# Optimization experiments

Hardware: AMD Instinct MI355X
Metric: run time of the kernel (lower is better)

## Reference

```python
import jax, jax.numpy as jnp
import numpy as np

N_NODES = 49
FEAT_DIM = 1280            # efficientnet_v2_s feature dim
NODE_DIM = FEAT_DIM // N_NODES  # 26
GAT_HID = 256
HEADS = 4
NUM_CLASSES = 5
BATCH = 8192


def _grid_edges():
    # 7x7 grid, 8-neighborhood, as in _create_grid_edges, plus PyG default self loops
    edges = []
    for i in range(7):
        for j in range(7):
            node = i * 7 + j
            for di in (-1, 0, 1):
                for dj in (-1, 0, 1):
                    if di == 0 and dj == 0:
                        continue
                    ni, nj = i + di, j + dj
                    if 0 <= ni < 7 and 0 <= nj < 7:
                        edges.append((node, ni * 7 + nj))
    edges += [(n, n) for n in range(N_NODES)]  # add_self_loops=True (PyG default)
    return np.asarray(edges, dtype=np.int64).T  # [2, 361]


def setup_inputs() -> dict:
    key = jax.random.key(0)
    ks = jax.random.split(key, 16)
    s = 0.05
    inp = {
        "x": jax.random.normal(ks[0], (BATCH, FEAT_DIM), jnp.float32),
        "transform_w": jax.random.normal(ks[1], (FEAT_DIM, N_NODES * NODE_DIM), jnp.float32) * s,
        "transform_b": jnp.zeros((N_NODES * NODE_DIM,), jnp.float32),
        # GATv2 layer 1: 26 -> 64 per head, 4 heads, concat -> 256
        "g1_wl": jax.random.normal(ks[2], (NODE_DIM, GAT_HID), jnp.float32) * s,
        "g1_wr": jax.random.normal(ks[3], (NODE_DIM, GAT_HID), jnp.float32) * s,
        "g1_att": jax.random.normal(ks[4], (HEADS, GAT_HID // HEADS), jnp.float32) * s,
        "g1_b": jnp.zeros((GAT_HID,), jnp.float32),
        # GATv2 layer 2: 256 -> 256, 1 head, mean
        "g2_wl": jax.random.normal(ks[5], (GAT_HID, GAT_HID), jnp.float32) * s,
        "g2_wr": jax.random.normal(ks[6], (GAT_HID, GAT_HID), jnp.float32) * s,
        "g2_att": jax.random.normal(ks[7], (1, GAT_HID), jnp.float32) * s,
        "g2_b": jnp.zeros((GAT_HID,), jnp.float32),
        "fc_w": jax.random.normal(ks[8], (NODE_DIM + GAT_HID, NUM_CLASSES), jnp.float32) * s,
        "fc_b": jnp.zeros((NUM_CLASSES,), jnp.float32),
        "edge_index": jnp.asarray(_grid_edges()),
    }
    return inp


def _gatv2(x, src, dst, wl, wr, att, b, heads, out_ch, concat):
    # PyG GATv2Conv (share_weights=False, negative_slope=0.2, eval mode)
    n = x.shape[0]
    xl = (x @ wl).reshape(n, heads, out_ch)  # source messages
    xr = (x @ wr).reshape(n, heads, out_ch)  # target side of attention
    e = jax.nn.leaky_relu(xl[src] + xr[dst], 0.2)        # [E, H, C]
    score = jnp.einsum('ehc,hc->eh', e, att)             # [E, H]
    smax = jax.ops.segment_max(score, dst, num_segments=n)
    ex = jnp.exp(score - smax[dst])
    den = jax.ops.segment_sum(ex, dst, num_segments=n)
    alpha = ex / den[dst]                                # softmax over in-edges per node
    out = jax.ops.segment_sum(xl[src] * alpha[..., None], dst, num_segments=n)  # [N,H,C]
    out = out.reshape(n, heads * out_ch) if concat else out.mean(axis=1)
    return out + b


def reference(x, transform_w, transform_b, g1_wl, g1_wr, g1_att, g1_b,
              g2_wl, g2_wr, g2_att, g2_b, fc_w, fc_b, edge_index):
    src, dst = edge_index[0], edge_index[1]
    node = (x @ transform_w + transform_b).reshape(-1, N_NODES, NODE_DIM)  # [B,49,26]

    def graph(nf):
        h = _gatv2(nf, src, dst, g1_wl, g1_wr, g1_att, g1_b, HEADS, GAT_HID // HEADS, True)
        h = jax.nn.elu(h)  # dropout inactive in eval
        h = _gatv2(h, src, dst, g2_wl, g2_wr, g2_att, g2_b, 1, GAT_HID, False)
        return h  # [49, 256]

    g = jax.vmap(graph)(node)                              # [B,49,256]
    pooled = jnp.concatenate([node, g], axis=-1).mean(axis=1)  # [B, 282]
    return pooled @ fc_w + fc_b
```

## Files before the change

### kernel.cpp

```cpp
#include <hip/hip_runtime.h>
#include <hip/hip_bf16.h>

typedef __bf16 bf16;
typedef __attribute__((ext_vector_type(8))) __bf16 bf16x8;
typedef __attribute__((ext_vector_type(4))) float f32x4;

constexpr int BATCH = 8192, NN = 49, ND = 26, NOUT = 1274, FD = 1280;
constexpr int HID = 256, NE = 361, HEADS = 4;
constexpr int KT_X = 40;
constexpr int MT_X = 512;
constexpr int NB_W = 10;
constexpr int NTB  = 9;

constexpr size_t OFF_XPACK = 0;
constexpr size_t SZ_XPACK  = (size_t)MT_X * KT_X * 512 * 2;
constexpr size_t OFF_WPACK = OFF_XPACK + SZ_XPACK;
constexpr size_t SZ_WPACK  = (size_t)NB_W * NTB * KT_X * 512 * 2;
constexpr size_t OFF_B1    = OFF_WPACK + SZ_WPACK;
constexpr size_t SZ_B1     = (size_t)32 * 512 * 2;
constexpr size_t OFF_B2    = OFF_B1 + SZ_B1;
constexpr size_t SZ_B2     = (size_t)32 * 8 * 512 * 2;
constexpr size_t OFF_N32   = OFF_B2 + SZ_B2;
constexpr size_t SZ_N32    = (size_t)BATCH * NN * 32 * 2;
constexpr size_t OFF_PN    = OFF_N32 + SZ_N32;
constexpr size_t SZ_PN     = (size_t)BATCH * ND * 4;
constexpr size_t OFF_CSR   = OFF_PN + SZ_PN;
constexpr size_t SZ_CSR    = 8192;
constexpr size_t OFF_CHUNK = OFF_CSR + SZ_CSR;


__global__ __launch_bounds__(256) void k_pack_x(const float* __restrict__ x,
                                                bf16* __restrict__ xp) {
    int g = blockIdx.x * 256 + threadIdx.x;
    int lane = g & 63, frag = g >> 6;
    int mt = frag / KT_X, kt = frag - mt * KT_X;
    int row = mt * 16 + (lane & 15);
    int k0  = kt * 32 + (lane >> 4) * 8;
    const float* src = x + (size_t)row * FD + k0;
    bf16x8 v;
#pragma unroll
    for (int j = 0; j < 8; ++j) v[j] = (bf16)src[j];
    *(bf16x8*)(xp + ((size_t)frag * 64 + lane) * 8) = v;
}

__global__ __launch_bounds__(256) void k_pack_w(const float* __restrict__ w,
                                                bf16* __restrict__ wp) {
    int g = blockIdx.x * 256 + threadIdx.x;
    int lane = g & 63, frag = g >> 6;
    int kt = frag % KT_X, t2 = frag / KT_X;
    int nt = t2 % NTB, nb = t2 / NTB;
    int col = nb * 130 + nt * 16 + (lane & 15);
    int k0  = kt * 32 + (lane >> 4) * 8;
    bool ok = (col < NOUT) && (col < nb * 130 + 130);
    bf16x8 v;
#pragma unroll
    for (int j = 0; j < 8; ++j)
        v[j] = ok ? (bf16)w[(size_t)(k0 + j) * NOUT + col] : (bf16)0.f;
    *(bf16x8*)(wp + ((size_t)frag * 64 + lane) * 8) = v;
}

__global__ __launch_bounds__(256) void k_pack_g1(const float* __restrict__ wl,
                                                 const float* __restrict__ wr,
                                                 bf16* __restrict__ bp) {
    int g = blockIdx.x * 256 + threadIdx.x;
    int lane = g & 63, nt = g >> 6;
    int n  = nt * 16 + (lane & 15);
    int k0 = (lane >> 4) * 8;
    bf16x8 v;
#pragma unroll
    for (int j = 0; j < 8; ++j) {
        int k = k0 + j;
        float f = 0.f;
        if (k < ND) f = (n < HID) ? wl[k * HID + n] : wr[k * HID + (n - HID)];
        v[j] = (bf16)f;
    }
    *(bf16x8*)(bp + ((size_t)nt * 64 + lane) * 8) = v;
}

__global__ __launch_bounds__(256) void k_pack_g2(const float* __restrict__ wl,
                                                 const float* __restrict__ wr,
                                                 bf16* __restrict__ bp) {
    int g = blockIdx.x * 256 + threadIdx.x;
    int lane = g & 63, frag = g >> 6;
    int nt = frag >> 3, kt = frag & 7;
    int n  = nt * 16 + (lane & 15);
    int k0 = kt * 32 + (lane >> 4) * 8;
    bf16x8 v;
#pragma unroll
    for (int j = 0; j < 8; ++j) {
        int k = k0 + j;
        float f = (n < HID) ? wl[k * HID + n] : wr[k * HID + (n - HID)];
        v[j] = (bf16)f;
    }
    *(bf16x8*)(bp + ((size_t)frag * 64 + lane) * 8) = v;
}

__global__ __launch_bounds__(128) void k_csr_par(const int* __restrict__ ei,
                                                 int* __restrict__ csr) {
    __shared__ int es[NE], ed[NE], cnt[NN], ocnt[NN], off[NN + 1], ooff[NN + 1];
    int tid = threadIdx.x;
    if (tid < NN) { cnt[tid] = 0; ocnt[tid] = 0; }
    for (int e = tid; e < NE; e += 128) { es[e] = ei[e]; ed[e] = ei[NE + e]; }
    __syncthreads();
    for (int e = tid; e < NE; e += 128) {
        atomicAdd(&cnt[ed[e]], 1);
        atomicAdd(&ocnt[es[e]], 1);
    }
    __syncthreads();
    if (tid == 0) {
        off[0] = 0; ooff[0] = 0;
        for (int n = 0; n < NN; ++n) {
            off[n + 1] = off[n] + cnt[n];
            ooff[n + 1] = ooff[n] + ocnt[n];
        }
    }
    __syncthreads();
    if (tid < NN) {
        int p = off[tid];
        for (int e = 0; e < NE; ++e)
            if (ed[e] == tid) { csr[50 + p] = e; csr[411 + p] = es[e]; ++p; }
    } else if (tid >= 64 && tid < 64 + NN) {
        int n = tid - 64;
        int p = ooff[n];
        for (int e = 0; e < NE; ++e)
            if (es[e] == n) { csr[822 + p] = e; ++p; }
    }
    if (tid < 50) { csr[tid] = off[tid]; csr[772 + tid] = ooff[tid]; }
}

__global__ __launch_bounds__(256, 2) void k_gemm_node(const bf16* __restrict__ xp,
                                                      const bf16* __restrict__ wp,
                                                      const float* __restrict__ tb,
                                                      bf16* __restrict__ node32) {
    __shared__ bf16 L[128][148];
    __shared__ float tbS[144];
    int tid = threadIdx.x, lane = tid & 63, w = tid >> 6;
    int nb = blockIdx.y, C0 = nb * 130;
    int mt0 = blockIdx.x * 16 + w * 4;
    if (tid < 144) { int col = C0 + tid; tbS[tid] = (col < NOUT) ? tb[col] : 0.f; }
    f32x4 acc[4][9] = {};
    const bf16* wpB = wp + (size_t)(nb * NTB) * KT_X * 512;
    for (int kt = 0; kt < KT_X; ++kt) {
        bf16x8 a[4];
#pragma unroll
        for (int i = 0; i < 4; ++i)
            a[i] = *(const bf16x8*)(xp + (((size_t)(mt0 + i) * KT_X + kt) * 64 + lane) * 8);
#pragma unroll
        for (int j = 0; j < NTB; ++j) {
            bf16x8 b = *(const bf16x8*)(wpB + ((size_t)(j * KT_X + kt) * 64 + lane) * 8);
#pragma unroll
            for (int i = 0; i < 4; ++i)
                acc[i][j] = __builtin_amdgcn_mfma_f32_16x16x32_bf16(a[i], b, acc[i][j], 0, 0, 0);
        }
    }
    int c0 = lane & 15, r0 = (lane >> 4) * 4;
    int nodes = (nb == 9) ? 4 : 5;
    int total = 128 * nodes * 4;
    for (int half = 0; half < 2; ++half) {
        __syncthreads();
        if ((w >> 1) == half) {
            int lrbase = (w & 1) * 64;
#pragma unroll
            for (int i = 0; i < 4; ++i) {
#pragma unroll
                for (int j = 0; j < NTB; ++j) {
                    int col = j * 16 + c0;
                    float bias = tbS[col];
#pragma unroll
                    for (int r = 0; r < 4; ++r)
                        L[lrbase + i * 16 + r0 + r][col] = (bf16)(acc[i][j][r] + bias);
                }
            }
        }
        __syncthreads();
        int B0 = blockIdx.x * 256 + half * 128;
        for (int t = tid; t < total; t += 256) {
            int q = t & 3, t2 = t >> 2;
            int n_l = t2 % nodes, brow = t2 / nodes;
            bf16x8 o;
#pragma unroll
            for (int jj = 0; jj < 8; ++jj) {
                int d = q * 8 + jj;
                o[jj] = (d < ND) ? L[brow][n_l * 26 + d] : (bf16)0.f;
            }
            *(bf16x8*)(node32 + (((size_t)(B0 + brow) * NN + nb * 5 + n_l) * 32 + q * 8)) = o;
        }
    }
}

__global__ __launch_bounds__(256) void k_pool(const bf16* __restrict__ node32,
                                              float* __restrict__ pN) {
    int b = blockIdx.x * 8 + (threadIdx.x >> 5);
    int d = threadIdx.x & 31;
    if (d >= ND) return;
    const bf16* base = node32 + (size_t)b * NN * 32 + d;
    float s = 0.f;
    for (int n = 0; n < NN; ++n) s += (float)base[n * 32];
    pN[b * ND + d] = s;
}

__global__ __launch_bounds__(512, 2) void k_fuse1(const bf16* __restrict__ n32,
                                                  const bf16* __restrict__ B1p,
                                                  bf16* __restrict__ h1f,
                                                  const float* __restrict__ att1,
                                                  const float* __restrict__ g1b,
                                                  const int* __restrict__ ei,
                                                  const int* __restrict__ csr) {
    __shared__ __align__(16) char X[NN * 1024];
    __shared__ __align__(16) float attS[256];
    __shared__ float sc[NE * 4], srden[NN * 4], bS[256];
    __shared__ int ieOff[50], ieId[NE], ieSrc[NE], srcS[NE], dstS[NE];

    int tid = threadIdx.x, lane = tid & 63, w = tid >> 6, g = blockIdx.x;

    for (int i = tid; i < 256; i += 512) { attS[i] = att1[i]; bS[i] = g1b[i]; }
    for (int i = tid; i < NE; i += 512) {
        srcS[i] = ei[i]; dstS[i] = ei[NE + i];
        ieId[i] = csr[50 + i]; ieSrc[i] = csr[411 + i];
    }
    if (tid < 50) ieOff[tid] = csr[tid];

    {
        int mt = w & 3, ng = w >> 2;
        int arow = mt * 16 + (lane & 15);
        bf16x8 a = {};
        if (arow < NN)
            a = *(const bf16x8*)(n32 + ((size_t)(g * NN + arow) * 32 + (lane >> 4) * 8));
        f32x4 acc[16];
#pragma unroll
        for (int j = 0; j < 16; ++j) {
            f32x4 z = {0.f, 0.f, 0.f, 0.f};
            bf16x8 b = *(const bf16x8*)(B1p + ((size_t)(ng * 16 + j) * 64 + lane) * 8);
            acc[j] = __builtin_amdgcn_mfma_f32_16x16x32_bf16(a, b, z, 0, 0, 0);
        }
        int c0 = lane & 15, r0 = (lane >> 4) * 4;
#pragma unroll
        for (int j = 0; j < 16; ++j) {
            int col = (ng * 16 + j) * 16 + c0;
#pragma unroll
            for (int r = 0; r < 4; ++r) {
                int n = mt * 16 + r0 + r;
                if (n < NN)
                    *(bf16*)(X + n * 1024 + ((col * 2) ^ ((n & 7) << 4))) = (bf16)acc[j][r];
            }
        }
    }
    __syncthreads();

    int rot = tid & 7;
    for (int task = tid; task < NE * 4; task += 512) {
        int h = task / NE, e = task - h * NE;
        int s = srcS[e], d = dstS[e];
        int sws = (s & 7) << 4, swd = (d & 7) << 4;
        const char* ps = X + s * 1024;
        const char* pd = X + d * 1024;
        float pa[4] = {0.f, 0.f, 0.f, 0.f};
#pragma unroll
        for (int i = 0; i < 8; ++i) {
            int cc = ((i + rot) & 7) * 8;
            bf16x8 xl = *(const bf16x8*)(ps + (((h * 64 + cc) * 2) ^ sws));
            bf16x8 xr = *(const bf16x8*)(pd + (((256 + h * 64 + cc) * 2) ^ swd));
            float4 a0 = *(const float4*)(attS + h * 64 + cc);
            float4 a1 = *(const float4*)(attS + h * 64 + cc + 4);
            const float aa[8] = {a0.x, a0.y, a0.z, a0.w, a1.x, a1.y, a1.z, a1.w};
#pragma unroll
            for (int q = 0; q < 8; ++q) {
                float v = (float)xl[q] + (float)xr[q];
                v = v > 0.f ? v : 0.2f * v;
                pa[q & 3] = fmaf(aa[q], v, pa[q & 3]);
            }
        }
        sc[e * 4 + h] = (pa[0] + pa[1]) + (pa[2] + pa[3]);
    }
    __syncthreads();
    for (int t = tid; t < NN * 4; t += 512) {
        int n = t >> 2, h = t & 3;
        float m = -1e30f;
        for (int j = ieOff[n]; j < ieOff[n + 1]; ++j) m = fmaxf(m, sc[ieId[j] * 4 + h]);
        float den = 0.f;
        for (int j = ieOff[n]; j < ieOff[n + 1]; ++j) {
            int idx = ieId[j] * 4 + h;
            float ex = __expf(sc[idx] - m);
            sc[idx] = ex; den += ex;
        }
        srden[t] = 1.f / den;
    }
    __syncthreads();
    for (int task = tid; task < NN * 32; task += 512) {
        int n = task >> 5, cb = task & 31;
        int ch0 = cb * 8, hh = cb >> 3;
        float a8[8] = {};
        int j0 = ieOff[n], j1 = ieOff[n + 1];
        for (int j = j0; j < j1; ++j) {
            float al = sc[ieId[j] * 4 + hh];
            int s = ieSrc[j];
            bf16x8 xv = *(const bf16x8*)(X + s * 1024 + ((ch0 * 2) ^ ((s & 7) << 4)));
#pragma unroll
            for (int q = 0; q < 8; ++q) a8[q] = fmaf(al, (float)xv[q], a8[q]);
        }
        float rs = srden[n * 4 + hh];
        bf16x8 o;
#pragma unroll
        for (int q = 0; q < 8; ++q) {
            float v = fmaf(a8[q], rs, bS[ch0 + q]);
            v = v > 0.f ? v : (__expf(v) - 1.f);
            o[q] = (bf16)v;
        }
        int Rl = g * NN + n;
        int kt = ch0 >> 5, kg = (ch0 >> 3) & 3;
        size_t addr = (((size_t)(Rl >> 4) * 8 + kt) * 64 + (Rl & 15) + 16 * kg) * 8;
        *(bf16x8*)(h1f + addr) = o;
    }
}

__global__ __launch_bounds__(256) void k_gemm_l2(const bf16* __restrict__ Af,
                                                 const bf16* __restrict__ Bf,
                                                 bf16* __restrict__ xlr) {
    __shared__ bf16 LT[128][136];
    int tid = threadIdx.x, lane = tid & 63, w = tid >> 6;
    int mtb = blockIdx.x * 8 + (w >> 1) * 4;
    int ntb = blockIdx.y * 8 + (w & 1) * 4;
    f32x4 acc[4][4] = {};
    for (int kt = 0; kt < 8; ++kt) {
        bf16x8 a[4], b[4];
#pragma unroll
        for (int i = 0; i < 4; ++i)
            a[i] = *(const bf16x8*)(Af + (((size_t)(mtb + i) * 8 + kt) * 64 + lane) * 8);
#pragma unroll
        for (int j = 0; j < 4; ++j)
            b[j] = *(const bf16x8*)(Bf + (((size_t)(ntb + j) * 8 + kt) * 64 + lane) * 8);
#pragma unroll
        for (int i = 0; i < 4; ++i)
#pragma unroll
            for (int j = 0; j < 4; ++j)
                acc[i][j] = __builtin_amdgcn_mfma_f32_16x16x32_bf16(a[i], b[j], acc[i][j], 0, 0, 0);
    }
    int c0 = lane & 15, r0 = (lane >> 4) * 4;
    int lr0 = (w >> 1) * 64, lc0 = (w & 1) * 64;
#pragma unroll
    for (int i = 0; i < 4; ++i)
#pragma unroll
        for (int j = 0; j < 4; ++j)
#pragma unroll
            for (int r = 0; r < 4; ++r)
                LT[lr0 + i * 16 + r0 + r][lc0 + j * 16 + c0] = (bf16)acc[i][j][r];
    __syncthreads();
    size_t R0 = (size_t)blockIdx.x * 128, C0 = (size_t)blockIdx.y * 128;
#pragma unroll
    for (int it = 0; it < 8; ++it) {
        int idx = (it * 256 + tid) * 8;
        int r = idx >> 7, c = idx & 127;
        bf16x8 v = *(const bf16x8*)&LT[r][c];
        *(bf16x8*)(xlr + (R0 + r) * 512 + C0 + c) = v;
    }
}

static __device__ __forceinline__ float waveReduceSum(float v) {
#pragma unroll
    for (int m = 32; m > 0; m >>= 1) v += __shfl_xor(v, m, 64);
    return v;
}

__global__ __launch_bounds__(512, 2) void k_edge2(const bf16* __restrict__ xlrG,
                                                  const float* __restrict__ pooledN,
                                                  const float* __restrict__ att2,
                                                  const float* __restrict__ g2b,
                                                  const float* __restrict__ fcw,
                                                  const float* __restrict__ fcb,
                                                  const int* __restrict__ ei,
                                                  const int* __restrict__ csr,
                                                  int graph_base,
                                                  float* __restrict__ out) {
    __shared__ __align__(16) char X[NN * 1024];
    __shared__ __align__(16) float attS[256];
    __shared__ float sc2[NE * 2], scE[NE], srdenN[NN], smaxN[NN], wS[NN];
    __shared__ float b2S[256], pA[256], pB[256], pool[288], fcwS[282 * 5];
    __shared__ int srcS[NE], dstS[NE], ieOff[50], ieId[NE], oOff[50], oId[NE];

    int tid = threadIdx.x, g = blockIdx.x;
    const char* srcp = (const char*)(xlrG + (size_t)g * NN * 512);
    for (int off = tid * 16; off < NN * 1024; off += 512 * 16) {
        int row = off >> 10;
        *(uint4*)(X + (off ^ ((row & 7) << 4))) = *(const uint4*)(srcp + off);
    }
    for (int i = tid; i < 256; i += 512) { attS[i] = att2[i]; b2S[i] = g2b[i]; }
    for (int i = tid; i < NE; i += 512) {
        srcS[i] = ei[i]; dstS[i] = ei[NE + i];
        ieId[i] = csr[50 + i]; oId[i] = csr[822 + i];
    }
    if (tid < 50) { ieOff[tid] = csr[tid]; oOff[tid] = csr[772 + tid]; }
    for (int i = tid; i < 282 * 5; i += 512) fcwS[i] = fcw[i];
    __syncthreads();

    int rot = tid & 7;
    for (int task = tid; task < NE * 2; task += 512) {
        int e = task >> 1, half = task & 1;
        int s = srcS[e], d = dstS[e];
        int sws = (s & 7) << 4, swd = (d & 7) << 4;
        const char* ps = X + s * 1024;
        const char* pd = X + d * 1024;
        float pa[4] = {0.f, 0.f, 0.f, 0.f};
#pragma unroll
        for (int i = 0; i < 16; ++i) {
            int cc = half * 128 + (((i + rot) & 15)) * 8;
            bf16x8 xl = *(const bf16x8*)(ps + ((cc * 2) ^ sws));
            bf16x8 xr = *(const bf16x8*)(pd + (((256 + cc) * 2) ^ swd));
            float4 a0 = *(const float4*)(attS + cc);
            float4 a1 = *(const float4*)(attS + cc + 4);
            const float aa[8] = {a0.x, a0.y, a0.z, a0.w, a1.x, a1.y, a1.z, a1.w};
#pragma unroll
            for (int q = 0; q < 8; ++q) {
                float v = (float)xl[q] + (float)xr[q];
                v = v > 0.f ? v : 0.2f * v;
                pa[q & 3] = fmaf(aa[q], v, pa[q & 3]);
            }
        }
        sc2[task] = (pa[0] + pa[1]) + (pa[2] + pa[3]);
    }
    __syncthreads();
    for (int e = tid; e < NE; e += 512) scE[e] = sc2[2 * e] + sc2[2 * e + 1];
    __syncthreads();
    for (int n = tid; n < NN; n += 512) {
        float m = -1e30f;
        for (int j = ieOff[n]; j < ieOff[n + 1]; ++j) m = fmaxf(m, scE[ieId[j]]);
        float den = 0.f;
        for (int j = ieOff[n]; j < ieOff[n + 1]; ++j) den += __expf(scE[ieId[j]] - m);
        smaxN[n] = m; srdenN[n] = 1.f / den;
    }
    __syncthreads();
    for (int n = tid; n < NN; n += 512) {
        float wacc = 0.f;
        for (int j = oOff[n]; j < oOff[n + 1]; ++j) {
            int e = oId[j], d = dstS[e];
            wacc += __expf(scE[e] - smaxN[d]) * srdenN[d];
        }
        wS[n] = wacc;
    }
    __syncthreads();
    {
        int ch = tid & 255, half = tid >> 8;
        int n0 = half ? 25 : 0, n1 = half ? NN : 25;
        float acc = 0.f;
        for (int n = n0; n < n1; ++n) {
            float v = (float)*(const bf16*)(X + n * 1024 + ((ch * 2) ^ ((n & 7) << 4)));
            acc = fmaf(wS[n], v, acc);
        }
        (half ? pB : pA)[ch] = acc;
    }
    __syncthreads();
    if (tid < ND) pool[tid] = pooledN[(size_t)(graph_base + g) * ND + tid] * (1.f / NN);
    else if (tid >= 32 && tid < 32 + HID) {
        int ch = tid - 32;
        pool[ND + ch] = (pA[ch] + pB[ch]) * (1.f / NN) + b2S[ch];
    }
    __syncthreads();
    int w5 = tid >> 6, lane = tid & 63;
    if (w5 < 5) {
        float a = 0.f;
        for (int d = lane; d < ND + HID; d += 64) a = fmaf(pool[d], fcwS[d * 5 + w5], a);
        a = waveReduceSum(a);
        if (lane == 0) out[(size_t)(graph_base + g) * 5 + w5] = a + fcb[w5];
    }
}

extern "C" void kernel_launch(void* const* d_in, const int* in_sizes, int n_in,
                              void* d_out, int out_size, void* d_ws, size_t ws_size,
                              hipStream_t stream) {
    const float* x   = (const float*)d_in[0];
    const float* tw  = (const float*)d_in[1];
    const float* tb  = (const float*)d_in[2];
    const float* wl1 = (const float*)d_in[3];
    const float* wr1 = (const float*)d_in[4];
    const float* at1 = (const float*)d_in[5];
    const float* b1  = (const float*)d_in[6];
    const float* wl2 = (const float*)d_in[7];
    const float* wr2 = (const float*)d_in[8];
    const float* at2 = (const float*)d_in[9];
    const float* b2  = (const float*)d_in[10];
    const float* fcw = (const float*)d_in[11];
    const float* fcb = (const float*)d_in[12];
    const int*   ei  = (const int*)d_in[13];
    float* out = (float*)d_out;

    char* ws = (char*)d_ws;
    bf16*  xp   = (bf16*)(ws + OFF_XPACK);
    bf16*  wp   = (bf16*)(ws + OFF_WPACK);
    bf16*  b1p  = (bf16*)(ws + OFF_B1);
    bf16*  b2p  = (bf16*)(ws + OFF_B2);
    bf16*  n32  = (bf16*)(ws + OFF_N32);
    float* pN   = (float*)(ws + OFF_PN);
    int*   csr  = (int*)(ws + OFF_CSR);

    int C = 512;
    for (int cand : {2048, 1024, 512}) {
        if (OFF_CHUNK + (size_t)cand * (50176 + 12544) <= ws_size) { C = cand; break; }
    }
    bf16* xlr = (bf16*)(ws + OFF_CHUNK);
    bf16* h1f = (bf16*)(ws + OFF_CHUNK + (size_t)C * 50176);
    int nchunks = BATCH / C;
    int MtC = C * NN / 16;

    k_pack_x<<<dim3(MT_X * KT_X * 64 / 256), dim3(256), 0, stream>>>(x, xp);
    k_pack_w<<<dim3(NB_W * NTB * KT_X * 64 / 256), dim3(256), 0, stream>>>(tw, wp);
    k_pack_g1<<<dim3(8), dim3(256), 0, stream>>>(wl1, wr1, b1p);
    k_pack_g2<<<dim3(64), dim3(256), 0, stream>>>(wl2, wr2, b2p);
    k_csr_par<<<dim3(1), dim3(128), 0, stream>>>(ei, csr);
    k_gemm_node<<<dim3(32, NB_W), dim3(256), 0, stream>>>(xp, wp, tb, n32);
    k_pool<<<dim3(BATCH / 8), dim3(256), 0, stream>>>(n32, pN);

    for (int c = 0; c < nchunks; ++c) {
        const bf16* n32c = n32 + (size_t)c * C * NN * 32;
        k_fuse1<<<dim3(C), dim3(512), 0, stream>>>(n32c, b1p, h1f, at1, b1, ei, csr);
        k_gemm_l2<<<dim3(MtC / 8, 4), dim3(256), 0, stream>>>(h1f, b2p, xlr);
        k_edge2<<<dim3(C), dim3(512), 0, stream>>>(xlr, pN, at2, b2, fcw, fcb,
                                                   ei, csr, c * C, out);
    }
}
```

Baseline: 1.068 ms.

## Split fused layer-2 edge kernel into score, softmax, weight and pool-FC kernels

Replaces the monolithic per-graph k_edge2 kernel, which staged 49 KB of node features in LDS and ran serial softmax loops, with four smaller kernels. Scores are read straight from global memory, softmax and per-node weights are spread across many threads over the whole chunk, and pooling with the FC layer runs in a light 256-thread kernel. The aim is to remove the large LDS footprint and the poorly parallel serial phases so occupancy rises. In exchange it adds extra launches per chunk, global round-trips for intermediates, and uncoalesced per-thread row reads in the score kernel.

After: 1.034 ms. 3.1% less time.

```diff
diff --git a/kernel.cpp b/kernel.cpp
--- a/kernel.cpp
+++ b/kernel.cpp
@@ -355,111 +355,105 @@
     }
 }
 
+__global__ __launch_bounds__(384) void k_score2(const bf16* __restrict__ xlr,
+                                                const float* __restrict__ att2,
+                                                const int* __restrict__ ei,
+                                                float* __restrict__ scE) {
+    __shared__ float attS[256];
+    int tid = threadIdx.x, g = blockIdx.x;
+    if (tid < 256) attS[tid] = att2[tid];
+    __syncthreads();
+    if (tid >= NE) return;
+    int s = ei[tid], d = ei[NE + tid];
+    const bf16* pl = xlr + ((size_t)g * NN + s) * 512;
+    const bf16* pr = xlr + ((size_t)g * NN + d) * 512 + 256;
+    float pa[4] = {0.f, 0.f, 0.f, 0.f};
+#pragma unroll 4
+    for (int i = 0; i < 32; ++i) {
+        bf16x8 xl = *(const bf16x8*)(pl + i * 8);
+        bf16x8 xr = *(const bf16x8*)(pr + i * 8);
+#pragma unroll
+        for (int q = 0; q < 8; ++q) {
+            float v = (float)xl[q] + (float)xr[q];
+            v = v > 0.f ? v : 0.2f * v;
+            pa[q & 3] = fmaf(attS[i * 8 + q], v, pa[q & 3]);
+        }
+    }
+    scE[(size_t)g * NE + tid] = (pa[0] + pa[1]) + (pa[2] + pa[3]);
+}
+
+__global__ __launch_bounds__(256) void k_soft2(const float* __restrict__ scE,
+                                               const int* __restrict__ csr,
+                                               float* __restrict__ sm,
+                                               float* __restrict__ sr, int C) {
+    int idx = blockIdx.x * 256 + threadIdx.x;
+    int g = idx / NN, n = idx - g * NN;
+    if (g >= C) return;
+    const float* sg = scE + (size_t)g * NE;
+    int j0 = csr[n], j1 = csr[n + 1];
+    float m = -1e30f;
+    for (int j = j0; j < j1; ++j) m = fmaxf(m, sg[csr[50 + j]]);
+    float den = 0.f;
+    for (int j = j0; j < j1; ++j) den += __expf(sg[csr[50 + j]] - m);
+    sm[idx] = m; sr[idx] = 1.f / den;
+}
+
+__global__ __launch_bounds__(256) void k_wn(const float* __restrict__ scE,
+                                            const int* __restrict__ csr,
+                                            const int* __restrict__ ei,
+                                            const float* __restrict__ sm,
+                                            const float* __restrict__ sr,
+                                            float* __restrict__ wN, int C) {
+    int idx = blockIdx.x * 256 + threadIdx.x;
+    int g = idx / NN, n = idx - g * NN;
+    if (g >= C) return;
+    const float* sg = scE + (size_t)g * NE;
+    const float* smg = sm + (size_t)g * NN;
+    const float* srg = sr + (size_t)g * NN;
+    float wa = 0.f;
+    int j0 = csr[772 + n], j1 = csr[772 + n + 1];
+    for (int j = j0; j < j1; ++j) {
+        int e = csr[822 + j];
+        int d = ei[NE + e];
+        wa += __expf(sg[e] - smg[d]) * srg[d];
+    }
+    wN[idx] = wa;
+}
+
 static __device__ __forceinline__ float waveReduceSum(float v) {
 #pragma unroll
     for (int m = 32; m > 0; m >>= 1) v += __shfl_xor(v, m, 64);
     return v;
 }
 
-__global__ __launch_bounds__(512, 2) void k_edge2(const bf16* __restrict__ xlrG,
-                                                  const float* __restrict__ pooledN,
-                                                  const float* __restrict__ att2,
-                                                  const float* __restrict__ g2b,
-                                                  const float* __restrict__ fcw,
-                                                  const float* __restrict__ fcb,
-                                                  const int* __restrict__ ei,
-                                                  const int* __restrict__ csr,
-                                                  int graph_base,
-                                                  float* __restrict__ out) {
-    __shared__ __align__(16) char X[NN * 1024];
-    __shared__ __align__(16) float attS[256];
-    __shared__ float sc2[NE * 2], scE[NE], srdenN[NN], smaxN[NN], wS[NN];
-    __shared__ float b2S[256], pA[256], pB[256], pool[288], fcwS[282 * 5];
-    __shared__ int srcS[NE], dstS[NE], ieOff[50], ieId[NE], oOff[50], oId[NE];
-
+__global__ __launch_bounds__(256) void k_poolfc(const bf16* __restrict__ xlr,
+                                                const float* __restrict__ wN,
+                                                const float* __restrict__ pN,
+                                                const float* __restrict__ g2b,
+                                                const float* __restrict__ fcw,
+                                                const float* __restrict__ fcb,
+                                                int graph_base,
+                                                float* __restrict__ out) {
+    __shared__ float wSs[NN];
+    __shared__ float poolS[288];
     int tid = threadIdx.x, g = blockIdx.x;
-    const char* srcp = (const char*)(xlrG + (size_t)g * NN * 512);
-    for (int off = tid * 16; off < NN * 1024; off += 512 * 16) {
-        int row = off >> 10;
-        *(uint4*)(X + (off ^ ((row & 7) << 4))) = *(const uint4*)(srcp + off);
-    }
-    for (int i = tid; i < 256; i += 512) { attS[i] = att2[i]; b2S[i] = g2b[i]; }
-    for (int i = tid; i < NE; i += 512) {
-        srcS[i] = ei[i]; dstS[i] = ei[NE + i];
-        ieId[i] = csr[50 + i]; oId[i] = csr[822 + i];
-    }
-    if (tid < 50) { ieOff[tid] = csr[tid]; oOff[tid] = csr[772 + tid]; }
-    for (int i = tid; i < 282 * 5; i += 512) fcwS[i] = fcw[i];
-    __syncthreads();
-
-    int rot = tid & 7;
-    for (int task = tid; task < NE * 2; task += 512) {
-        int e = task >> 1, half = task & 1;
-        int s = srcS[e], d = dstS[e];
-        int sws = (s & 7) << 4, swd = (d & 7) << 4;
-        const char* ps = X + s * 1024;
-        const char* pd = X + d * 1024;
-        float pa[4] = {0.f, 0.f, 0.f, 0.f};
-#pragma unroll
-        for (int i = 0; i < 16; ++i) {
-            int cc = half * 128 + (((i + rot) & 15)) * 8;
-            bf16x8 xl = *(const bf16x8*)(ps + ((cc * 2) ^ sws));
-            bf16x8 xr = *(const bf16x8*)(pd + (((256 + cc) * 2) ^ swd));
-            float4 a0 = *(const float4*)(attS + cc);
-            float4 a1 = *(const float4*)(attS + cc + 4);
-            const float aa[8] = {a0.x, a0.y, a0.z, a0.w, a1.x, a1.y, a1.z, a1.w};
-#pragma unroll
-            for (int q = 0; q < 8; ++q) {
-                float v = (float)xl[q] + (float)xr[q];
-                v = v > 0.f ? v : 0.2f * v;
-                pa[q & 3] = fmaf(aa[q], v, pa[q & 3]);
-            }
-        }
-        sc2[task] = (pa[0] + pa[1]) + (pa[2] + pa[3]);
-    }
-    __syncthreads();
-    for (int e = tid; e < NE; e += 512) scE[e] = sc2[2 * e] + sc2[2 * e + 1];
-    __syncthreads();
-    for (int n = tid; n < NN; n += 512) {
-        float m = -1e30f;
-        for (int j = ieOff[n]; j < ieOff[n + 1]; ++j) m = fmaxf(m, scE[ieId[j]]);
-        float den = 0.f;
-        for (int j = ieOff[n]; j < ieOff[n + 1]; ++j) den += __expf(scE[ieId[j]] - m);
-        smaxN[n] = m; srdenN[n] = 1.f / den;
-    }
-    __syncthreads();
-    for (int n = tid; n < NN; n += 512) {
-        float wacc = 0.f;
-        for (int j = oOff[n]; j < oOff[n + 1]; ++j) {
-            int e = oId[j], d = dstS[e];
-            wacc += __expf(scE[e] - smaxN[d]) * srdenN[d];
-        }
-        wS[n] = wacc;
-    }
+    if (tid < NN) wSs[tid] = wN[(size_t)g * NN + tid];
+    if (tid >= 64 && tid < 64 + ND)
+        poolS[tid - 64] = pN[(size_t)(graph_base + g) * ND + (tid - 64)] * (1.f / NN);
     __syncthreads();
     {
-        int ch = tid & 255, half = tid >> 8;
-        int n0 = half ? 25 : 0, n1 = half ? NN : 25;
+        const bf16* base = xlr + (size_t)g * NN * 512 + tid;
         float acc = 0.f;
-        for (int n = n0; n < n1; ++n) {
-            float v = (float)*(const bf16*)(X + n * 1024 + ((ch * 2) ^ ((n & 7) << 4)));
-            acc = fmaf(wS[n], v, acc);
-        }
-        (half ? pB : pA)[ch] = acc;
-    }
-    __syncthreads();
-    if (tid < ND) pool[tid] = pooledN[(size_t)(graph_base + g) * ND + tid] * (1.f / NN);
-    else if (tid >= 32 && tid < 32 + HID) {
-        int ch = tid - 32;
-        pool[ND + ch] = (pA[ch] + pB[ch]) * (1.f / NN) + b2S[ch];
+        for (int n = 0; n < NN; ++n) acc = fmaf(wSs[n], (float)base[n * 512], acc);
+        poolS[ND + tid] = acc * (1.f / NN) + g2b[tid];
     }
     __syncthreads();
     int w5 = tid >> 6, lane = tid & 63;
-    if (w5 < 5) {
+    for (int o = w5; o < 5; o += 4) {
         float a = 0.f;
-        for (int d = lane; d < ND + HID; d += 64) a = fmaf(pool[d], fcwS[d * 5 + w5], a);
+        for (int d = lane; d < ND + HID; d += 64) a = fmaf(poolS[d], fcw[d * 5 + o], a);
         a = waveReduceSum(a);
-        if (lane == 0) out[(size_t)(graph_base + g) * 5 + w5] = a + fcb[w5];
+        if (lane == 0) out[(size_t)(graph_base + g) * 5 + o] = a + fcb[o];
     }
 }
 
@@ -491,14 +485,20 @@
     float* pN   = (float*)(ws + OFF_PN);
     int*   csr  = (int*)(ws + OFF_CSR);
 
+    const size_t perC = 50176 + 12544 + 1444 + 3 * 196;
     int C = 512;
     for (int cand : {2048, 1024, 512}) {
-        if (OFF_CHUNK + (size_t)cand * (50176 + 12544) <= ws_size) { C = cand; break; }
-    }
-    bf16* xlr = (bf16*)(ws + OFF_CHUNK);
-    bf16* h1f = (bf16*)(ws + OFF_CHUNK + (size_t)C * 50176);
+        if (OFF_CHUNK + (size_t)cand * perC <= ws_size) { C = cand; break; }
+    }
+    bf16*  xlr = (bf16*)(ws + OFF_CHUNK);
+    bf16*  h1f = (bf16*)(ws + OFF_CHUNK + (size_t)C * 50176);
+    float* scE = (float*)(ws + OFF_CHUNK + (size_t)C * (50176 + 12544));
+    float* smB = scE + (size_t)C * NE;
+    float* srB = smB + (size_t)C * NN;
+    float* wNB = srB + (size_t)C * NN;
     int nchunks = BATCH / C;
     int MtC = C * NN / 16;
+    int gnBlocks = (C * NN + 255) / 256;
 
     k_pack_x<<<dim3(MT_X * KT_X * 64 / 256), dim3(256), 0, stream>>>(x, xp);
     k_pack_w<<<dim3(NB_W * NTB * KT_X * 64 / 256), dim3(256), 0, stream>>>(tw, wp);
@@ -512,7 +512,10 @@
         const bf16* n32c = n32 + (size_t)c * C * NN * 32;
         k_fuse1<<<dim3(C), dim3(512), 0, stream>>>(n32c, b1p, h1f, at1, b1, ei, csr);
         k_gemm_l2<<<dim3(MtC / 8, 4), dim3(256), 0, stream>>>(h1f, b2p, xlr);
-        k_edge2<<<dim3(C), dim3(512), 0, stream>>>(xlr, pN, at2, b2, fcw, fcb,
-                                                   ei, csr, c * C, out);
-    }
-}
+        k_score2<<<dim3(C), dim3(384), 0, stream>>>(xlr, at2, ei, scE);
+        k_soft2<<<dim3(gnBlocks), dim3(256), 0, stream>>>(scE, csr, smB, srB, C);
+        k_wn<<<dim3(gnBlocks), dim3(256), 0, stream>>>(scE, csr, ei, smB, srB, wNB, C);
+        k_poolfc<<<dim3(C), dim3(256), 0, stream>>>(xlr, wNB, pN, b2, fcw, fcb,
+                                                    c * C, out);
+    }
+}
```
